# Optimization experiments

Hardware: AMD Instinct MI355X
Metric: run time of the kernel (lower is better)

The kernel has to match this reference:

```python
import jax, jax.numpy as jnp
import numpy as np

N_NODES = 100000
N_EDGES = 1600000
D_IN = 128
D_HID = 128
N_CLS = 16
N_GRAPHS = 64


def setup_inputs() -> dict:
    key = jax.random.key(0)
    ks = jax.random.split(key, 12)
    h = jax.random.normal(ks[0], (N_NODES, D_IN), dtype=jnp.float32)
    src = jax.random.randint(ks[1], (N_EDGES,), 0, N_NODES, dtype=jnp.int32)
    dst = jax.random.randint(ks[2], (N_EDGES,), 0, N_NODES, dtype=jnp.int32)
    graph_ids = jnp.sort(jax.random.randint(ks[3], (N_NODES,), 0, N_GRAPHS, dtype=jnp.int32))
    s = 1.0 / np.sqrt(D_IN)
    W1_self = jax.random.uniform(ks[4], (D_IN, D_HID), jnp.float32, -s, s)
    W1_neigh = jax.random.uniform(ks[5], (D_IN, D_HID), jnp.float32, -s, s)
    b1 = jnp.zeros((D_HID,), jnp.float32)
    s2 = 1.0 / np.sqrt(D_HID)
    W2_self = jax.random.uniform(ks[6], (D_HID, D_HID), jnp.float32, -s2, s2)
    W2_neigh = jax.random.uniform(ks[7], (D_HID, D_HID), jnp.float32, -s2, s2)
    b2 = jnp.zeros((D_HID,), jnp.float32)
    Wc = jax.random.uniform(ks[8], (D_HID, N_CLS), jnp.float32, -s2, s2)
    bc = jnp.zeros((N_CLS,), jnp.float32)
    return {"h": h, "src": src, "dst": dst, "graph_ids": graph_ids, "num_graphs": N_GRAPHS,
            "W1_self": W1_self, "W1_neigh": W1_neigh, "b1": b1,
            "W2_self": W2_self, "W2_neigh": W2_neigh, "b2": b2,
            "Wc": Wc, "bc": bc}


def _sage_conv(h, src, dst, W_self, W_neigh, b):
    # DGL SAGEConv 'mean': out = fc_self(h) + fc_neigh(mean of in-neighbor feats) + bias
    n = h.shape[0]
    msg = jnp.take(h, src, axis=0)                               # [E, d] gather
    agg = jax.ops.segment_sum(msg, dst, num_segments=n)          # [N, d] scatter-add
    deg = jax.ops.segment_sum(jnp.ones((src.shape[0],), h.dtype), dst, num_segments=n)
    neigh = agg / jnp.maximum(deg, 1.0)[:, None]                 # mean, zero-degree safe
    return h @ W_self + neigh @ W_neigh + b


def reference(h, src, dst, graph_ids, num_graphs,
              W1_self, W1_neigh, b1, W2_self, W2_neigh, b2, Wc, bc):
    x = jax.nn.relu(_sage_conv(h, src, dst, W1_self, W1_neigh, b1))
    x = _sage_conv(x, src, dst, W2_self, W2_neigh, b2)
    # dgl.mean_nodes: per-graph mean over node features
    gsum = jax.ops.segment_sum(x, graph_ids, num_segments=num_graphs)    # [G, d]
    gcnt = jax.ops.segment_sum(jnp.ones((x.shape[0],), x.dtype), graph_ids, num_segments=num_graphs)
    hg = gsum / jnp.maximum(gcnt, 1.0)[:, None]
    return hg @ Wc + bc                                                  # [G, num_classes]
```

## Files before the change

kernel.cpp:

```cpp
#include <hip/hip_runtime.h>

#define D        128
#define N_GRAPHS 64
#define N_CLS    16
#define LDA      40
#define SLOTS    48
#define CAP      8192

typedef unsigned int   uint;
typedef unsigned short ushort;
typedef __attribute__((ext_vector_type(8))) short short8;
typedef __attribute__((ext_vector_type(4))) float f32x4;

__device__ inline ushort f2b(float f) {
    uint u = __float_as_uint(f);
    u += 0x7fffu + ((u >> 16) & 1u);
    return (ushort)(u >> 16);
}

__device__ __forceinline__ int swzi(int row, int col) {
    return row * 256 + (col ^ (((row >> 3) & 7) << 3));
}


__global__ __launch_bounds__(256) void k_boot(
    const float* __restrict__ h, ushort* __restrict__ fb,
    const float* __restrict__ Ws, const float* __restrict__ Wn,
    ushort* __restrict__ wT,
    const int* __restrict__ gid, int* __restrict__ gstart,
    const int* __restrict__ src, const int* __restrict__ dst,
    int* __restrict__ bcount, uint* __restrict__ ebuf,
    int E, int NB, int N, int t4) {
    __shared__ int hist[512], base[512], lcur[512];
    int bb = blockIdx.x;
    int t  = threadIdx.x;

    if (bb < 256) {
        int per = (E + 255) / 256;
        int e0 = bb * per;
        int e1 = min(e0 + per, E);
        for (int i = t; i < NB; i += 256) { hist[i] = 0; lcur[i] = 0; }
        __syncthreads();
        for (int e = e0 + t; e < e1; e += 256) atomicAdd(&hist[dst[e] >> 8], 1);
        __syncthreads();
        for (int i = t; i < NB; i += 256)
            base[i] = hist[i] ? atomicAdd(&bcount[i], hist[i]) : 0;
        __syncthreads();
        for (int e = e0 + t; e < e1; e += 256) {
            int dd = dst[e];
            int b = dd >> 8;
            int off = atomicAdd(&lcur[b], 1);
            int pos = base[b] + off;
            if (pos < CAP)
                ebuf[(size_t)b * CAP + pos] = ((uint)src[e] << 8) | (uint)(dd & 255);
        }
    } else if (bb < 384) {
        int i = (bb - 256) * 256 + t;
        int c = i >> 8, k = i & 255;
        float v = (k < 128) ? Ws[k * 128 + c] : Wn[(k - 128) * 128 + c];
        wT[c * 256 + k] = f2b(v);
    } else if (bb == 384) {
        int g = t;
        if (g <= N_GRAPHS) {
            int lo = 0, hi = N;
            while (lo < hi) {
                int mid = (lo + hi) >> 1;
                if (gid[mid] < g) lo = mid + 1; else hi = mid;
            }
            gstart[g] = lo;
        }
    } else {
        int i = (bb - 385) * 256 + t;
        if (i < t4) {
            float4 v = ((const float4*)h)[i];
            ushort4 o;
            o.x = f2b(v.x); o.y = f2b(v.y); o.z = f2b(v.z); o.w = f2b(v.w);
            ((ushort4*)fb)[i] = o;
        }
    }
}


__global__ __launch_bounds__(1024) void k_bucket(
    const uint* __restrict__ ebuf, const int* __restrict__ bcount,
    int* __restrict__ csrf, int* __restrict__ deg, float* __restrict__ invdeg,
    int N) {
    __shared__ int ldeg[256];
    __shared__ int lcsr[256 * SLOTS];
    int b = blockIdx.x, t = threadIdx.x;
    if (t < 256) ldeg[t] = 0;
    __syncthreads();
    int cnt = bcount[b];
    if (cnt > CAP) cnt = CAP;
    const uint* __restrict__ eb = ebuf + (size_t)b * CAP;
    for (int i = t; i < cnt; i += 1024) {
        uint r = eb[i];
        int dl = r & 255;
        int sl = atomicAdd(&ldeg[dl], 1);
        if (sl < SLOTS) lcsr[dl * SLOTS + sl] = (int)(r >> 8);
    }
    __syncthreads();
    int n0 = b << 8;
    int lim = (N - n0) * SLOTS;
    if (lim > 256 * SLOTS) lim = 256 * SLOTS;
    for (int i = t; i < lim; i += 1024)
        csrf[(size_t)n0 * SLOTS + i] = lcsr[i];
    if (t < 256 && n0 + t < N) {
        int d = ldeg[t];
        deg[n0 + t] = d;
        invdeg[n0 + t] = 1.0f / (float)(d > 1 ? d : 1);
    }
}


__global__ __launch_bounds__(256) void k_aggb(
    const ushort* __restrict__ fb, const int* __restrict__ deg,
    const int* __restrict__ csrf, const float* __restrict__ invdeg,
    ushort* __restrict__ outb, int N) {
    int lane = threadIdx.x & 63;
    int n = blockIdx.x * 4 + (threadIdx.x >> 6);
    if (n >= N) return;
    int d = deg[n];
    if (d > SLOTS) d = SLOTS;
    const int* __restrict__ lst = csrf + (size_t)n * SLOTS;
    int ej = lane >> 4;
    int cg = lane & 15;

    float acc[8];
#pragma unroll
    for (int i = 0; i < 8; i++) acc[i] = 0.f;

    int e = ej;
    for (; e + 4 < d; e += 8) {
        int s0 = lst[e];
        int s1 = lst[e + 4];
        uint4 v0 = *(const uint4*)(fb + (size_t)s0 * D + cg * 8);
        uint4 v1 = *(const uint4*)(fb + (size_t)s1 * D + cg * 8);
        acc[0] += __uint_as_float(v0.x << 16);
        acc[1] += __uint_as_float(v0.x & 0xffff0000u);
        acc[2] += __uint_as_float(v0.y << 16);
        acc[3] += __uint_as_float(v0.y & 0xffff0000u);
        acc[4] += __uint_as_float(v0.z << 16);
        acc[5] += __uint_as_float(v0.z & 0xffff0000u);
        acc[6] += __uint_as_float(v0.w << 16);
        acc[7] += __uint_as_float(v0.w & 0xffff0000u);
        acc[0] += __uint_as_float(v1.x << 16);
        acc[1] += __uint_as_float(v1.x & 0xffff0000u);
        acc[2] += __uint_as_float(v1.y << 16);
        acc[3] += __uint_as_float(v1.y & 0xffff0000u);
        acc[4] += __uint_as_float(v1.z << 16);
        acc[5] += __uint_as_float(v1.z & 0xffff0000u);
        acc[6] += __uint_as_float(v1.w << 16);
        acc[7] += __uint_as_float(v1.w & 0xffff0000u);
    }
    for (; e < d; e += 4) {
        int s = lst[e];
        uint4 v = *(const uint4*)(fb + (size_t)s * D + cg * 8);
        acc[0] += __uint_as_float(v.x << 16);
        acc[1] += __uint_as_float(v.x & 0xffff0000u);
        acc[2] += __uint_as_float(v.y << 16);
        acc[3] += __uint_as_float(v.y & 0xffff0000u);
        acc[4] += __uint_as_float(v.z << 16);
        acc[5] += __uint_as_float(v.z & 0xffff0000u);
        acc[6] += __uint_as_float(v.w << 16);
        acc[7] += __uint_as_float(v.w & 0xffff0000u);
    }
#pragma unroll
    for (int i = 0; i < 8; i++) {
        acc[i] += __shfl_xor(acc[i], 16);
        acc[i] += __shfl_xor(acc[i], 32);
    }
    if (ej == 0) {
        float id = invdeg[n];
        uint4 o;
        o.x = (uint)f2b(acc[0] * id) | ((uint)f2b(acc[1] * id) << 16);
        o.y = (uint)f2b(acc[2] * id) | ((uint)f2b(acc[3] * id) << 16);
        o.z = (uint)f2b(acc[4] * id) | ((uint)f2b(acc[5] * id) << 16);
        o.w = (uint)f2b(acc[6] * id) | ((uint)f2b(acc[7] * id) << 16);
        *(uint4*)(outb + (size_t)n * D + cg * 8) = o;
    }
}


__global__ __launch_bounds__(256, 2) void k_mmp2(
    const ushort* __restrict__ hb, const ushort* __restrict__ nbb,
    const ushort* __restrict__ wT, const float* __restrict__ b,
    ushort* __restrict__ x1b, int N, int MMB,
    const int* __restrict__ src, const int* __restrict__ dst,
    const int* __restrict__ gid, const int* __restrict__ deg,
    int* __restrict__ bcount2, uint* __restrict__ ebuf2, int E, int NB) {
    __shared__ __align__(16) ushort As[128 * LDA];
    __shared__ __align__(16) ushort Bs[128 * LDA];
    __shared__ int hist[512], base[512], lcur[512];

    if (blockIdx.x >= MMB) {
        int bb = blockIdx.x - MMB;
        int t = threadIdx.x;
        int per = (E + 255) / 256;
        int e0 = bb * per;
        int e1 = min(e0 + per, E);
        for (int i = t; i < NB; i += 256) { hist[i] = 0; lcur[i] = 0; }
        __syncthreads();
        for (int e = e0 + t; e < e1; e += 256) atomicAdd(&hist[src[e] >> 8], 1);
        __syncthreads();
        for (int i = t; i < NB; i += 256)
            base[i] = hist[i] ? atomicAdd(&bcount2[i], hist[i]) : 0;
        __syncthreads();
        for (int e = e0 + t; e < e1; e += 256) {
            int ss = src[e];
            int dd = dst[e];
            int bk = ss >> 8;
            int off = atomicAdd(&lcur[bk], 1);
            int pos = base[bk] + off;
            if (pos < CAP) {
                int g  = gid[dd];
                int dc = deg[dd]; if (dc > 127) dc = 127;
                ebuf2[(size_t)bk * CAP + pos] =
                    (uint)(ss & 255) | ((uint)g << 8) | ((uint)dc << 14);
            }
        }
        return;
    }

    int t    = threadIdx.x;
    int w    = t >> 6;
    int lane = t & 63;
    int m    = lane & 15;
    int quad = lane >> 4;
    int n0   = blockIdx.x * 128;

    f32x4 acc[2][8];
#pragma unroll
    for (int rt = 0; rt < 2; rt++)
#pragma unroll
        for (int ct = 0; ct < 8; ct++) acc[rt][ct] = (f32x4){0.f, 0.f, 0.f, 0.f};

#pragma unroll 1
    for (int kc = 0; kc < 8; kc++) {
        int k0 = kc * 32;
        const ushort* __restrict__ A = (k0 < 128) ? hb : nbb;
        int ka = k0 & 127;
        __syncthreads();
#pragma unroll
        for (int i = 0; i < 2; i++) {
            int linear = i * 256 + t;
            int row = linear >> 2;
            int q   = linear & 3;
            int nn = n0 + row;
            uint4 v = make_uint4(0u, 0u, 0u, 0u);
            if (nn < N) v = *(const uint4*)(A + (size_t)nn * D + ka + q * 8);
            *(uint4*)(&As[row * LDA + q * 8]) = v;
        }
#pragma unroll
        for (int i = 0; i < 2; i++) {
            int linear = i * 256 + t;
            int col = linear >> 2;
            int q   = linear & 3;
            uint4 v = *(const uint4*)(wT + (size_t)col * 256 + k0 + q * 8);
            *(uint4*)(&Bs[col * LDA + q * 8]) = v;
        }
        __syncthreads();
        short8 af[2], bf[8];
#pragma unroll
        for (int rt = 0; rt < 2; rt++)
            af[rt] = *(const short8*)(&As[(w * 32 + rt * 16 + m) * LDA + quad * 8]);
#pragma unroll
        for (int ct = 0; ct < 8; ct++)
            bf[ct] = *(const short8*)(&Bs[(ct * 16 + m) * LDA + quad * 8]);
#pragma unroll
        for (int rt = 0; rt < 2; rt++)
#pragma unroll
            for (int ct = 0; ct < 8; ct++)
                acc[rt][ct] = __builtin_amdgcn_mfma_f32_16x16x32_bf16(
                    af[rt], bf[ct], acc[rt][ct], 0, 0, 0);
    }
#pragma unroll
    for (int ct = 0; ct < 8; ct++) {
        float bias = b[ct * 16 + m];
#pragma unroll
        for (int rt = 0; rt < 2; rt++) {
#pragma unroll
            for (int r = 0; r < 4; r++) {
                int n = n0 + w * 32 + rt * 16 + quad * 4 + r;
                if (n < N)
                    x1b[(size_t)n * D + ct * 16 + m] =
                        f2b(fmaxf(acc[rt][ct][r] + bias, 0.f));
            }
        }
    }
}


__global__ __launch_bounds__(256, 1) void k_wg(
    const uint* __restrict__ ebuf2, const int* __restrict__ bcount2,
    const ushort* __restrict__ x1b, const int* __restrict__ gstart,
    float* __restrict__ S1, float* __restrict__ S2, int N, int WSB) {
    __shared__ __align__(16) char smem[131072];

    if (blockIdx.x >= WSB) {
        int b2 = blockIdx.x - WSB;
        int g  = b2 >> 3;
        int ch = b2 & 7;
        int r0 = gstart[g], r1 = gstart[g + 1];
        int len = r1 - r0;
        if (len <= 0) return;
        int L = (len + 7) >> 3;
        int a = r0 + ch * L;
        int bnd = min(a + L, r1);
        if (a >= bnd) return;
        int rp = threadIdx.x >> 6;
        int cp = threadIdx.x & 63;
        float ax = 0.f, ay = 0.f;
        const uint* __restrict__ M = (const uint*)x1b;
        for (int n = a + rp; n < bnd; n += 4) {
            uint v = M[(size_t)n * 64 + cp];
            ax += __uint_as_float(v << 16);
            ay += __uint_as_float(v & 0xffff0000u);
        }
        atomicAdd(&S1[g * D + cp * 2], ax);
        atomicAdd(&S1[g * D + cp * 2 + 1], ay);
        return;
    }

    float*  lwcT = (float*)smem;
    ushort* lxT  = (ushort*)smem;
    ushort* lwcb = (ushort*)(smem + 65536);
    ushort* lwlo = (ushort*)(smem + 98304);

    int b = blockIdx.x, t = threadIdx.x;
    int n0 = b << 8;

    for (int i = t; i < 16384; i += 256) lwcT[i] = 0.f;
    __syncthreads();

    int cnt = bcount2[b];
    if (cnt > CAP) cnt = CAP;
    const uint* __restrict__ eb = ebuf2 + (size_t)b * CAP;
    for (int i = t; i < cnt; i += 256) {
        uint r = eb[i];
        int sl = (int)(r & 255u);
        int g  = (int)((r >> 8) & 63u);
        int dc = (int)((r >> 14) & 127u);
        float id = 1.0f / (float)(dc > 1 ? dc : 1);
        atomicAdd(&lwcT[g * 256 + sl], id);
    }
    __syncthreads();

    for (int i = t; i < 16384; i += 256) {
        int g = i >> 8, sl = i & 255;
        float v = lwcT[i];
        ushort hi = f2b(v);
        float fhi = __uint_as_float((uint)hi << 16);
        ushort lo = f2b(v - fhi);
        int si = swzi(g, sl);
        lwcb[si] = hi;
        lwlo[si] = lo;
    }
    __syncthreads();

    const uint4* __restrict__ x4 = (const uint4*)x1b;
#pragma unroll 1
    for (int it = 0; it < 16; ++it) {
        int l = it * 256 + t;
        int n = l >> 4, q = l & 15;
        uint4 v = make_uint4(0u, 0u, 0u, 0u);
        int nn = n0 + n;
        if (nn < N) v = x4[(size_t)nn * 16 + q];
        int d0 = q * 8;
        lxT[swzi(d0 + 0, n)] = (ushort)(v.x & 0xffffu);
        lxT[swzi(d0 + 1, n)] = (ushort)(v.x >> 16);
        lxT[swzi(d0 + 2, n)] = (ushort)(v.y & 0xffffu);
        lxT[swzi(d0 + 3, n)] = (ushort)(v.y >> 16);
        lxT[swzi(d0 + 4, n)] = (ushort)(v.z & 0xffffu);
        lxT[swzi(d0 + 5, n)] = (ushort)(v.z >> 16);
        lxT[swzi(d0 + 6, n)] = (ushort)(v.w & 0xffffu);
        lxT[swzi(d0 + 7, n)] = (ushort)(v.w >> 16);
    }
    __syncthreads();

    int wv = t >> 6, lane = t & 63, m = lane & 15, quad = lane >> 4;
    f32x4 acc[8];
#pragma unroll
    for (int dt = 0; dt < 8; ++dt) acc[dt] = (f32x4){0.f, 0.f, 0.f, 0.f};

#pragma unroll 1
    for (int k8 = 0; k8 < 8; ++k8) {
        int kc = k8 * 32 + quad * 8;
        int ar = wv * 16 + m;
        short8 ahi = *(const short8*)&lwcb[swzi(ar, kc)];
        short8 alo = *(const short8*)&lwlo[swzi(ar, kc)];
#pragma unroll
        for (int dt = 0; dt < 8; ++dt) {
            short8 bfr = *(const short8*)&lxT[swzi(dt * 16 + m, kc)];
            acc[dt] = __builtin_amdgcn_mfma_f32_16x16x32_bf16(alo, bfr, acc[dt], 0, 0, 0);
            acc[dt] = __builtin_amdgcn_mfma_f32_16x16x32_bf16(ahi, bfr, acc[dt], 0, 0, 0);
        }
    }
#pragma unroll
    for (int dt = 0; dt < 8; ++dt) {
#pragma unroll
        for (int r = 0; r < 4; ++r) {
            int g = wv * 16 + quad * 4 + r;
            atomicAdd(&S2[g * 128 + dt * 16 + m], acc[dt][r]);
        }
    }
}


__global__ void k_final(const float* __restrict__ S1, const float* __restrict__ S2,
                        const int* __restrict__ gstart, const float* __restrict__ W2s,
                        const float* __restrict__ W2n, const float* __restrict__ b2,
                        const float* __restrict__ Wc, const float* __restrict__ bc,
                        float* __restrict__ out) {
    __shared__ float s1[D], s2[D], hg[D];
    int g = blockIdx.x, c = threadIdx.x;
    s1[c] = S1[g * D + c];
    s2[c] = S2[g * D + c];
    __syncthreads();
    float acc = 0.f;
#pragma unroll 8
    for (int k = 0; k < D; k++) {
        acc = fmaf(s1[k], W2s[k * D + c], acc);
        acc = fmaf(s2[k], W2n[k * D + c], acc);
    }
    int cnt = gstart[g + 1] - gstart[g];
    hg[c] = (cnt > 0) ? (acc / (float)cnt + b2[c]) : 0.f;
    __syncthreads();
    if (c < N_CLS) {
        float o = bc[c];
        for (int k = 0; k < D; k++) o = fmaf(hg[k], Wc[k * N_CLS + c], o);
        out[g * N_CLS + c] = o;
    }
}


extern "C" void kernel_launch(void* const* d_in, const int* in_sizes, int n_in,
                              void* d_out, int out_size, void* d_ws, size_t ws_size,
                              hipStream_t stream) {
    const float* h   = (const float*)d_in[0];
    const int*   src = (const int*)d_in[1];
    const int*   dst = (const int*)d_in[2];
    const int*   gid = (const int*)d_in[3];
    const float* W1s = (const float*)d_in[5];
    const float* W1n = (const float*)d_in[6];
    const float* b1  = (const float*)d_in[7];
    const float* W2s = (const float*)d_in[8];
    const float* W2n = (const float*)d_in[9];
    const float* b2  = (const float*)d_in[10];
    const float* Wc  = (const float*)d_in[11];
    const float* bc  = (const float*)d_in[12];
    float* out = (float*)d_out;

    const int N = in_sizes[0] / D;
    const int E = in_sizes[1];
    const int NB = (N + 255) >> 8;

    char* w = (char*)d_ws;
    size_t off = 0;
    auto alloc = [&](size_t elems) -> void* {
        void* p = w + off;
        off += elems * 4;
        return p;
    };
    float* S1      = (float*)alloc((size_t)N_GRAPHS * D);
    float* S2      = (float*)alloc((size_t)N_GRAPHS * D);
    int*   bcount  = (int*)alloc(512);
    int*   bcount2 = (int*)alloc(512);
    size_t zero_bytes = off;
    int*   deg    = (int*)alloc(N);
    float* invdeg = (float*)alloc(N);
    int*   gstart = (int*)alloc(128);
    int*   csrf   = (int*)alloc((size_t)N * SLOTS);
    ushort* fb    = (ushort*)alloc((size_t)N * 64);
    ushort* nbb   = (ushort*)alloc((size_t)N * 64);
    ushort* x1b   = (ushort*)alloc((size_t)N * 64);
    ushort* wT    = (ushort*)alloc(16384);
    uint*  ebuf  = (uint*)nbb;
    uint*  ebuf2 = (uint*)csrf;
    (void)ws_size;

    hipMemsetAsync(d_ws, 0, zero_bytes, stream);

    int t4 = N * 32;
    int CB = (t4 + 255) / 256;
    int MMB = (N + 127) / 128;

    k_boot<<<256 + 128 + 1 + CB, 256, 0, stream>>>(
        h, fb, W1s, W1n, wT, gid, gstart, src, dst, bcount, ebuf, E, NB, N, t4);
    k_bucket<<<NB, 1024, 0, stream>>>(ebuf, bcount, csrf, deg, invdeg, N);
    k_aggb<<<(N + 3) / 4, 256, 0, stream>>>(fb, deg, csrf, invdeg, nbb, N);
    k_mmp2<<<MMB + 256, 256, 0, stream>>>(
        fb, nbb, wT, b1, x1b, N, MMB, src, dst, gid, deg, bcount2, ebuf2, E, NB);
    k_wg<<<NB + N_GRAPHS * 8, 256, 0, stream>>>(
        ebuf2, bcount2, x1b, gstart, S1, S2, N, NB);
    k_final<<<N_GRAPHS, 128, 0, stream>>>(S1, S2, gstart, W2s, W2n, b2, Wc, bc, out);
}
```

Baseline: 357.7 us.

## Widen k_wg to 1024 threads and replace S2 atomics with per-block partials

k_wg now runs 16 waves per block, and each wave computes a 16x32 tile of the graph-by-feature product instead of 16x128, so fewer MFMA accumulators are needed per thread. The atomicAdd of the S2 results is replaced by plain stores of per-block partials into a buffer that reuses fb, and k_final sums those partials across blocks. The per-graph S1 sum uses 2 chunks of 1024 threads instead of 8 chunks of 256, and the LDS swizzle changes to xor in the low row bits. This removes global atomic contention, at the cost of an extra partial buffer to read in k_final and 128KB of LDS per block, which limits occupancy.

```diff
diff --git a/kernel.cpp b/kernel.cpp
--- a/kernel.cpp
+++ b/kernel.cpp
@@ -18,8 +18,8 @@
     return (ushort)(u >> 16);
 }
 
-__device__ __forceinline__ int swzi(int row, int col) {
-    return row * 256 + (col ^ (((row >> 3) & 7) << 3));
+__device__ __forceinline__ int swz2i(int row, int col) {
+    return row * 256 + (col ^ (((row ^ (row >> 3)) & 7) << 3));
 }
 
 
@@ -291,20 +291,20 @@
 }
 
 
-__global__ __launch_bounds__(256, 1) void k_wg(
+__global__ __launch_bounds__(1024, 4) void k_wg(
     const uint* __restrict__ ebuf2, const int* __restrict__ bcount2,
     const ushort* __restrict__ x1b, const int* __restrict__ gstart,
-    float* __restrict__ S1, float* __restrict__ S2, int N, int WSB) {
+    float* __restrict__ S1, float* __restrict__ P, int N, int WSB) {
     __shared__ __align__(16) char smem[131072];
 
     if (blockIdx.x >= WSB) {
         int b2 = blockIdx.x - WSB;
-        int g  = b2 >> 3;
-        int ch = b2 & 7;
+        int g  = b2 >> 1;
+        int ch = b2 & 1;
         int r0 = gstart[g], r1 = gstart[g + 1];
         int len = r1 - r0;
         if (len <= 0) return;
-        int L = (len + 7) >> 3;
+        int L = (len + 1) >> 1;
         int a = r0 + ch * L;
         int bnd = min(a + L, r1);
         if (a >= bnd) return;
@@ -312,7 +312,7 @@
         int cp = threadIdx.x & 63;
         float ax = 0.f, ay = 0.f;
         const uint* __restrict__ M = (const uint*)x1b;
-        for (int n = a + rp; n < bnd; n += 4) {
+        for (int n = a + rp; n < bnd; n += 16) {
             uint v = M[(size_t)n * 64 + cp];
             ax += __uint_as_float(v << 16);
             ay += __uint_as_float(v & 0xffff0000u);
@@ -330,13 +330,13 @@
     int b = blockIdx.x, t = threadIdx.x;
     int n0 = b << 8;
 
-    for (int i = t; i < 16384; i += 256) lwcT[i] = 0.f;
+    for (int i = t; i < 16384; i += 1024) lwcT[i] = 0.f;
     __syncthreads();
 
     int cnt = bcount2[b];
     if (cnt > CAP) cnt = CAP;
     const uint* __restrict__ eb = ebuf2 + (size_t)b * CAP;
-    for (int i = t; i < cnt; i += 256) {
+    for (int i = t; i < cnt; i += 1024) {
         uint r = eb[i];
         int sl = (int)(r & 255u);
         int g  = (int)((r >> 8) & 63u);
@@ -346,13 +346,13 @@
     }
     __syncthreads();
 
-    for (int i = t; i < 16384; i += 256) {
+    for (int i = t; i < 16384; i += 1024) {
         int g = i >> 8, sl = i & 255;
         float v = lwcT[i];
         ushort hi = f2b(v);
         float fhi = __uint_as_float((uint)hi << 16);
         ushort lo = f2b(v - fhi);
-        int si = swzi(g, sl);
+        int si = swz2i(g, sl);
         lwcb[si] = hi;
         lwlo[si] = lo;
     }
@@ -360,76 +360,95 @@
 
     const uint4* __restrict__ x4 = (const uint4*)x1b;
 #pragma unroll 1
-    for (int it = 0; it < 16; ++it) {
-        int l = it * 256 + t;
+    for (int it = 0; it < 4; ++it) {
+        int l = it * 1024 + t;
         int n = l >> 4, q = l & 15;
         uint4 v = make_uint4(0u, 0u, 0u, 0u);
         int nn = n0 + n;
         if (nn < N) v = x4[(size_t)nn * 16 + q];
         int d0 = q * 8;
-        lxT[swzi(d0 + 0, n)] = (ushort)(v.x & 0xffffu);
-        lxT[swzi(d0 + 1, n)] = (ushort)(v.x >> 16);
-        lxT[swzi(d0 + 2, n)] = (ushort)(v.y & 0xffffu);
-        lxT[swzi(d0 + 3, n)] = (ushort)(v.y >> 16);
-        lxT[swzi(d0 + 4, n)] = (ushort)(v.z & 0xffffu);
-        lxT[swzi(d0 + 5, n)] = (ushort)(v.z >> 16);
-        lxT[swzi(d0 + 6, n)] = (ushort)(v.w & 0xffffu);
-        lxT[swzi(d0 + 7, n)] = (ushort)(v.w >> 16);
+        lxT[swz2i(d0 + 0, n)] = (ushort)(v.x & 0xffffu);
+        lxT[swz2i(d0 + 1, n)] = (ushort)(v.x >> 16);
+        lxT[swz2i(d0 + 2, n)] = (ushort)(v.y & 0xffffu);
+        lxT[swz2i(d0 + 3, n)] = (ushort)(v.y >> 16);
+        lxT[swz2i(d0 + 4, n)] = (ushort)(v.z & 0xffffu);
+        lxT[swz2i(d0 + 5, n)] = (ushort)(v.z >> 16);
+        lxT[swz2i(d0 + 6, n)] = (ushort)(v.w & 0xffffu);
+        lxT[swz2i(d0 + 7, n)] = (ushort)(v.w >> 16);
     }
     __syncthreads();
 
     int wv = t >> 6, lane = t & 63, m = lane & 15, quad = lane >> 4;
-    f32x4 acc[8];
-#pragma unroll
-    for (int dt = 0; dt < 8; ++dt) acc[dt] = (f32x4){0.f, 0.f, 0.f, 0.f};
+    int s  = wv & 3;
+    int hs = wv >> 2;
+    f32x4 acc[2];
+    acc[0] = (f32x4){0.f, 0.f, 0.f, 0.f};
+    acc[1] = (f32x4){0.f, 0.f, 0.f, 0.f};
 
 #pragma unroll 1
     for (int k8 = 0; k8 < 8; ++k8) {
         int kc = k8 * 32 + quad * 8;
-        int ar = wv * 16 + m;
-        short8 ahi = *(const short8*)&lwcb[swzi(ar, kc)];
-        short8 alo = *(const short8*)&lwlo[swzi(ar, kc)];
-#pragma unroll
-        for (int dt = 0; dt < 8; ++dt) {
-            short8 bfr = *(const short8*)&lxT[swzi(dt * 16 + m, kc)];
-            acc[dt] = __builtin_amdgcn_mfma_f32_16x16x32_bf16(alo, bfr, acc[dt], 0, 0, 0);
-            acc[dt] = __builtin_amdgcn_mfma_f32_16x16x32_bf16(ahi, bfr, acc[dt], 0, 0, 0);
-        }
-    }
-#pragma unroll
-    for (int dt = 0; dt < 8; ++dt) {
+        int ar = s * 16 + m;
+        short8 ahi = *(const short8*)&lwcb[swz2i(ar, kc)];
+        short8 alo = *(const short8*)&lwlo[swz2i(ar, kc)];
+#pragma unroll
+        for (int d2 = 0; d2 < 2; ++d2) {
+            short8 bfr = *(const short8*)&lxT[swz2i(hs * 32 + d2 * 16 + m, kc)];
+            acc[d2] = __builtin_amdgcn_mfma_f32_16x16x32_bf16(alo, bfr, acc[d2], 0, 0, 0);
+            acc[d2] = __builtin_amdgcn_mfma_f32_16x16x32_bf16(ahi, bfr, acc[d2], 0, 0, 0);
+        }
+    }
+    float* __restrict__ Pb = P + (size_t)b * 8192;
+#pragma unroll
+    for (int d2 = 0; d2 < 2; ++d2) {
 #pragma unroll
         for (int r = 0; r < 4; ++r) {
-            int g = wv * 16 + quad * 4 + r;
-            atomicAdd(&S2[g * 128 + dt * 16 + m], acc[dt][r]);
-        }
-    }
-}
-
-
-__global__ void k_final(const float* __restrict__ S1, const float* __restrict__ S2,
-                        const int* __restrict__ gstart, const float* __restrict__ W2s,
-                        const float* __restrict__ W2n, const float* __restrict__ b2,
-                        const float* __restrict__ Wc, const float* __restrict__ bc,
-                        float* __restrict__ out) {
-    __shared__ float s1[D], s2[D], hg[D];
-    int g = blockIdx.x, c = threadIdx.x;
-    s1[c] = S1[g * D + c];
-    s2[c] = S2[g * D + c];
-    __syncthreads();
-    float acc = 0.f;
+            int g = s * 16 + quad * 4 + r;
+            Pb[g * 128 + hs * 32 + d2 * 16 + m] = acc[d2][r];
+        }
+    }
+}
+
+
+__global__ __launch_bounds__(256) void k_final(
+    const float* __restrict__ S1, const float* __restrict__ P, int NBLK,
+    const int* __restrict__ gstart, const float* __restrict__ W2s,
+    const float* __restrict__ W2n, const float* __restrict__ b2,
+    const float* __restrict__ Wc, const float* __restrict__ bc,
+    float* __restrict__ out) {
+    __shared__ float s1[D], s2[2][D], hg[D];
+    int g = blockIdx.x, t = threadIdx.x;
+    int c = t & 127, hh = t >> 7;
+    const float* __restrict__ Pg = P + (size_t)g * 128 + c;
+    float a0 = 0.f, a1 = 0.f, a2 = 0.f, a3 = 0.f;
+    int bb = hh;
+    for (; bb + 6 < NBLK; bb += 8) {
+        a0 += Pg[(size_t)bb * 8192];
+        a1 += Pg[(size_t)(bb + 2) * 8192];
+        a2 += Pg[(size_t)(bb + 4) * 8192];
+        a3 += Pg[(size_t)(bb + 6) * 8192];
+    }
+    for (; bb < NBLK; bb += 2) a0 += Pg[(size_t)bb * 8192];
+    s2[hh][c] = a0 + a1 + a2 + a3;
+    if (hh == 0) s1[c] = S1[g * D + c];
+    __syncthreads();
+    if (t < 128) s2[0][c] += s2[1][c];
+    __syncthreads();
+    if (t < 128) {
+        float acc = 0.f;
 #pragma unroll 8
-    for (int k = 0; k < D; k++) {
-        acc = fmaf(s1[k], W2s[k * D + c], acc);
-        acc = fmaf(s2[k], W2n[k * D + c], acc);
-    }
-    int cnt = gstart[g + 1] - gstart[g];
-    hg[c] = (cnt > 0) ? (acc / (float)cnt + b2[c]) : 0.f;
-    __syncthreads();
-    if (c < N_CLS) {
-        float o = bc[c];
-        for (int k = 0; k < D; k++) o = fmaf(hg[k], Wc[k * N_CLS + c], o);
-        out[g * N_CLS + c] = o;
+        for (int k = 0; k < D; k++) {
+            acc = fmaf(s1[k], W2s[k * D + c], acc);
+            acc = fmaf(s2[0][k], W2n[k * D + c], acc);
+        }
+        int cnt = gstart[g + 1] - gstart[g];
+        hg[c] = (cnt > 0) ? (acc / (float)cnt + b2[c]) : 0.f;
+    }
+    __syncthreads();
+    if (t < N_CLS) {
+        float o = bc[t];
+        for (int k = 0; k < D; k++) o = fmaf(hg[k], Wc[k * N_CLS + t], o);
+        out[g * N_CLS + t] = o;
     }
 }
 
@@ -463,7 +482,6 @@
         return p;
     };
     float* S1      = (float*)alloc((size_t)N_GRAPHS * D);
-    float* S2      = (float*)alloc((size_t)N_GRAPHS * D);
     int*   bcount  = (int*)alloc(512);
     int*   bcount2 = (int*)alloc(512);
     size_t zero_bytes = off;
@@ -477,6 +495,7 @@
     ushort* wT    = (ushort*)alloc(16384);
     uint*  ebuf  = (uint*)nbb;
     uint*  ebuf2 = (uint*)csrf;
+    float* P     = (float*)fb;
     (void)ws_size;
 
     hipMemsetAsync(d_ws, 0, zero_bytes, stream);
@@ -491,7 +510,8 @@
     k_aggb<<<(N + 3) / 4, 256, 0, stream>>>(fb, deg, csrf, invdeg, nbb, N);
     k_mmp2<<<MMB + 256, 256, 0, stream>>>(
         fb, nbb, wT, b1, x1b, N, MMB, src, dst, gid, deg, bcount2, ebuf2, E, NB);
-    k_wg<<<NB + N_GRAPHS * 8, 256, 0, stream>>>(
-        ebuf2, bcount2, x1b, gstart, S1, S2, N, NB);
-    k_final<<<N_GRAPHS, 128, 0, stream>>>(S1, S2, gstart, W2s, W2n, b2, Wc, bc, out);
-}
+    k_wg<<<NB + 128, 1024, 0, stream>>>(
+        ebuf2, bcount2, x1b, gstart, S1, P, N, NB);
+    k_final<<<N_GRAPHS, 256, 0, stream>>>(
+        S1, P, NB, gstart, W2s, W2n, b2, Wc, bc, out);
+}
```

Result: faster. 334.4 us (-6.5%).
